# Optimization experiments

Measured on AMD Instinct MI355X. Metric: run time of the kernel, lower is better.

## Reference

```python
import jax, jax.numpy as jnp
import numpy as np

N_NODES = 100000
N_FEATURES = 128
N_FILTERS = 128
N_EDGES = 3200000


def setup_inputs() -> dict:
    key = jax.random.key(0)
    k_x, k_f, k_src, k_dst, k_w = jax.random.split(key, 5)
    x = jax.random.normal(k_x, (N_NODES, N_FEATURES), dtype=jnp.float32)
    filters = jax.random.normal(k_f, (N_FEATURES, N_FILTERS), dtype=jnp.float32)
    edge_src = jax.random.randint(k_src, (N_EDGES,), 0, N_NODES, dtype=jnp.int64)
    edge_dst = jnp.sort(jax.random.randint(k_dst, (N_EDGES,), 0, N_NODES, dtype=jnp.int64))
    edge_weight = jax.random.uniform(k_w, (N_EDGES,), dtype=jnp.float32)
    return {"x": x, "filters": filters, "edge_src": edge_src,
            "edge_dst": edge_dst, "edge_weight": edge_weight}


def reference(x, filters, edge_src, edge_dst, edge_weight):
    # Dense feature transform: XF = x @ filters  -> [N, n_filters]
    XF = jnp.matmul(x, filters)
    # Sparse aggregation: out[d] += w_e * XF[s] for each edge (s, d, w_e)
    # equivalent to torch.sparse.mm(transform, XF) with transform in COO form.
    msgs = XF[edge_src] * edge_weight[:, None]           # [E, n_filters]
    out = jax.ops.segment_sum(msgs, edge_dst, num_segments=N_NODES)
    return out
```

## Files before the change

### kernel.cpp

```cpp
#include <hip/hip_runtime.h>
#include <stdint.h>

#define N_NODES 100000
#define N_FEAT 128
#define N_EDGES 3200000

static __device__ __forceinline__ unsigned int f2bf_u(float f) {
    unsigned int u = __float_as_uint(f);
    u += 0x7FFFu + ((u >> 16) & 1u);
    return u >> 16;
}

typedef __bf16 bf16x8 __attribute__((ext_vector_type(8)));
typedef float f32x4 __attribute__((ext_vector_type(4)));

__global__ __launch_bounds__(256) void k_prep(
        const float* __restrict__ x, unsigned short* __restrict__ xi8,
        float* __restrict__ xscale,
        const float* __restrict__ f, unsigned short* __restrict__ fT,
        const int* __restrict__ dst, int* __restrict__ row_ptr) {
    int b = blockIdx.x;
    if (b < 25000) {
        int wave = threadIdx.x >> 6, lane = threadIdx.x & 63;
        int node = b * 4 + wave;
        float2 v = *(const float2*)(x + (size_t)node * 128 + lane * 2);
        float am = fmaxf(fabsf(v.x), fabsf(v.y));
        for (int d = 1; d < 64; d <<= 1) am = fmaxf(am, __shfl_xor(am, d));
        float s = am * (1.f / 127.f);
        float inv = 127.f / fmaxf(am, 1e-20f);
        int q0 = (int)rintf(v.x * inv), q1 = (int)rintf(v.y * inv);
        xi8[(size_t)node * 64 + lane] =
            (unsigned short)((q0 & 0xFF) | ((q1 & 0xFF) << 8));
        if (lane == 0) xscale[node] = s;
    } else if (b < 37500) {
        int e = (b - 25000) * 256 + threadIdx.x;
        if (e >= N_EDGES) return;
        int dcur = dst[e];
        if (e == 0) {
            for (int d = 0; d <= dcur; ++d) row_ptr[d] = 0;
        } else {
            int dprev = dst[e - 1];
            for (int d = dprev + 1; d <= dcur; ++d) row_ptr[d] = e;
        }
        if (e == N_EDGES - 1) {
            for (int d = dcur + 1; d <= N_NODES; ++d) row_ptr[d] = N_EDGES;
        }
    } else {
        int i = (b - 37500) * 256 + threadIdx.x;
        if (i >= N_FEAT * N_FEAT) return;
        int k = i >> 7, n = i & 127;
        fT[n * N_FEAT + k] = (unsigned short)f2bf_u(f[i]);
    }
}

__global__ __launch_bounds__(256) void k_aggregate(
        const unsigned int* __restrict__ xi8,
        const float* __restrict__ xscale,
        const int* __restrict__ src,
        const float* __restrict__ w,
        const int* __restrict__ row_ptr,
        unsigned int* __restrict__ aggb) {
    __shared__ uint2 smeta[4][64];
    int wave = threadIdx.x >> 6, lane = threadIdx.x & 63;
    int node = blockIdx.x * 4 + wave;
    if (node >= N_NODES) return;
    int half = lane >> 5, f = lane & 31;
    int start = row_ptr[node], end = row_ptr[node + 1];
    float a0 = 0.f, a1 = 0.f, a2 = 0.f, a3 = 0.f;

    for (int e0 = start; e0 < end; e0 += 64) {
        int e = e0 + lane;
        uint2 m = make_uint2(0u, 0u);
        if (e < end) {
            int sv = src[e];
            m.x = (unsigned int)sv;
            m.y = __float_as_uint(w[e] * xscale[sv]);
        }
        smeta[wave][lane] = m;
        int cnt16 = (min(64, end - e0) + 15) & ~15;
        for (int j = 0; j < cnt16; j += 16) {
            unsigned int vv[8]; float wj[8];
#pragma unroll
            for (int u = 0; u < 8; ++u) {
                uint2 mm = smeta[wave][j + u * 2 + half];
                wj[u] = __uint_as_float(mm.y);
                vv[u] = xi8[mm.x * 32 + f];
            }
#pragma unroll
            for (int u = 0; u < 8; ++u) {
                int s32 = (int)vv[u];
                a0 = fmaf(wj[u], (float)((s32 << 24) >> 24), a0);
                a1 = fmaf(wj[u], (float)((s32 << 16) >> 24), a1);
                a2 = fmaf(wj[u], (float)((s32 <<  8) >> 24), a2);
                a3 = fmaf(wj[u], (float)( s32        >> 24), a3);
            }
        }
    }
    a0 += __shfl_xor(a0, 32);
    a1 += __shfl_xor(a1, 32);
    a2 += __shfl_xor(a2, 32);
    a3 += __shfl_xor(a3, 32);
    if (half == 0) {
        uint2 o;
        o.x = (f2bf_u(a1) << 16) | f2bf_u(a0);
        o.y = (f2bf_u(a3) << 16) | f2bf_u(a2);
        *(uint2*)(aggb + (size_t)node * 64 + f * 2) = o;
    }
}

#define LDA 136

__global__ __launch_bounds__(256, 2) void k_gemm(
        const unsigned short* __restrict__ A,
        const unsigned short* __restrict__ BT,
        float* __restrict__ C) {
    __shared__ unsigned short Abuf[128 * LDA];
    __shared__ unsigned short Bbuf[128 * LDA];
    int t = threadIdx.x;
    int tileM = blockIdx.x * 128;

    for (int i = 0; i < 8; ++i) {
        int c = t + i * 256;
        int r = c >> 4, c8 = c & 15;
        int grow = tileM + r;
        if (grow >= N_NODES) grow = N_NODES - 1;
        uint4 va = *(const uint4*)(A + (long long)grow * 128 + c8 * 8);
        *(uint4*)(Abuf + r * LDA + c8 * 8) = va;
        uint4 vb = *(const uint4*)(BT + r * 128 + c8 * 8);
        *(uint4*)(Bbuf + r * LDA + c8 * 8) = vb;
    }
    __syncthreads();

    int wave = t >> 6, lane = t & 63;
    int wm = (wave >> 1) * 64, wn = (wave & 1) * 64;
    int m15 = lane & 15, q = lane >> 4;

    f32x4 acc[4][4];
    for (int i = 0; i < 4; ++i)
        for (int j = 0; j < 4; ++j)
            acc[i][j] = f32x4{0.f, 0.f, 0.f, 0.f};

    for (int kk = 0; kk < 128; kk += 32) {
        bf16x8 a[4], b[4];
        for (int i = 0; i < 4; ++i)
            a[i] = *(const bf16x8*)(Abuf + (wm + i * 16 + m15) * LDA + kk + q * 8);
        for (int j = 0; j < 4; ++j)
            b[j] = *(const bf16x8*)(Bbuf + (wn + j * 16 + m15) * LDA + kk + q * 8);
        for (int i = 0; i < 4; ++i)
            for (int j = 0; j < 4; ++j)
                acc[i][j] = __builtin_amdgcn_mfma_f32_16x16x32_bf16(a[i], b[j], acc[i][j], 0, 0, 0);
    }

    for (int i = 0; i < 4; ++i) {
        int rowbase = tileM + wm + i * 16 + q * 4;
        for (int j = 0; j < 4; ++j) {
            int col = wn + j * 16 + m15;
            for (int r = 0; r < 4; ++r) {
                int grow = rowbase + r;
                if (grow < N_NODES)
                    C[(long long)grow * 128 + col] = acc[i][j][r];
            }
        }
    }
}

extern "C" void kernel_launch(void* const* d_in, const int* in_sizes, int n_in,
                              void* d_out, int out_size, void* d_ws, size_t ws_size,
                              hipStream_t stream) {
    const float* x        = (const float*)d_in[0];
    const float* filters  = (const float*)d_in[1];
    const int*   edge_src = (const int*)d_in[2];
    const int*   edge_dst = (const int*)d_in[3];
    const float* edge_w   = (const float*)d_in[4];
    float* out = (float*)d_out;

    char* ws = (char*)d_ws;
    unsigned short* xi8   = (unsigned short*)(ws);
    float*          xsc   = (float*)        (ws + 13ll * 1024 * 1024);
    unsigned int*   aggb  = (unsigned int*) (ws + 14ll * 1024 * 1024);
    unsigned short* fT    = (unsigned short*)(ws + 40ll * 1024 * 1024);
    int*            rp    = (int*)          (ws + 41ll * 1024 * 1024);

    hipLaunchKernelGGL(k_prep, dim3(37564), dim3(256), 0, stream,
                       x, xi8, xsc, filters, fT, edge_dst, rp);
    hipLaunchKernelGGL(k_aggregate, dim3(25000), dim3(256), 0, stream,
                       (const unsigned int*)xi8, xsc, edge_src, edge_w, rp, aggb);
    hipLaunchKernelGGL(k_gemm, dim3(782), dim3(256), 0, stream,
                       (const unsigned short*)aggb, fT, out);
}
```

Measured before the change: 210.4 us.

## Fuse sparse aggregation with bf16 GEMM in one kernel via LDS staging

Merges the aggregation and the GEMM into one kernel. Each 512-thread block aggregates 64 nodes into a bf16 tile kept in LDS, multiplies it by the filter matrix with MFMA, and writes fp32 output through an LDS-staged, coalesced float4 store. This removes the global round trip of the aggregated intermediate and one kernel launch. The quantize prep now handles two nodes per wave with float4 loads. The cost is fewer, larger blocks, each of which must finish gathering before its GEMM starts, so occupancy and latency hiding during the gather phase may drop.

Result: slower. 232.2 us (+10.4%).

```diff
diff --git a/kernel.cpp b/kernel.cpp
--- a/kernel.cpp
+++ b/kernel.cpp
@@ -15,25 +15,27 @@
 typedef float f32x4 __attribute__((ext_vector_type(4)));
 
 __global__ __launch_bounds__(256) void k_prep(
-        const float* __restrict__ x, unsigned short* __restrict__ xi8,
+        const float* __restrict__ x, unsigned int* __restrict__ xi8,
         float* __restrict__ xscale,
         const float* __restrict__ f, unsigned short* __restrict__ fT,
         const int* __restrict__ dst, int* __restrict__ row_ptr) {
     int b = blockIdx.x;
-    if (b < 25000) {
+    if (b < 12500) {
         int wave = threadIdx.x >> 6, lane = threadIdx.x & 63;
-        int node = b * 4 + wave;
-        float2 v = *(const float2*)(x + (size_t)node * 128 + lane * 2);
-        float am = fmaxf(fabsf(v.x), fabsf(v.y));
-        for (int d = 1; d < 64; d <<= 1) am = fmaxf(am, __shfl_xor(am, d));
+        int l32 = lane & 31;
+        int node = b * 8 + wave * 2 + (lane >> 5);
+        float4 v = *(const float4*)(x + (size_t)node * 128 + l32 * 4);
+        float am = fmaxf(fmaxf(fabsf(v.x), fabsf(v.y)), fmaxf(fabsf(v.z), fabsf(v.w)));
+        for (int d = 1; d < 32; d <<= 1) am = fmaxf(am, __shfl_xor(am, d));
         float s = am * (1.f / 127.f);
         float inv = 127.f / fmaxf(am, 1e-20f);
         int q0 = (int)rintf(v.x * inv), q1 = (int)rintf(v.y * inv);
-        xi8[(size_t)node * 64 + lane] =
-            (unsigned short)((q0 & 0xFF) | ((q1 & 0xFF) << 8));
-        if (lane == 0) xscale[node] = s;
-    } else if (b < 37500) {
-        int e = (b - 25000) * 256 + threadIdx.x;
+        int q2 = (int)rintf(v.z * inv), q3 = (int)rintf(v.w * inv);
+        xi8[(size_t)node * 32 + l32] = (unsigned int)((q0 & 0xFF) | ((q1 & 0xFF) << 8) |
+                                                      ((q2 & 0xFF) << 16) | ((q3 & 0xFF) << 24));
+        if (l32 == 0) xscale[node] = s;
+    } else if (b < 25000) {
+        int e = (b - 12500) * 256 + threadIdx.x;
         if (e >= N_EDGES) return;
         int dcur = dst[e];
         if (e == 0) {
@@ -46,121 +48,111 @@
             for (int d = dcur + 1; d <= N_NODES; ++d) row_ptr[d] = N_EDGES;
         }
     } else {
-        int i = (b - 37500) * 256 + threadIdx.x;
+        int i = (b - 25000) * 256 + threadIdx.x;
         if (i >= N_FEAT * N_FEAT) return;
         int k = i >> 7, n = i & 127;
         fT[n * N_FEAT + k] = (unsigned short)f2bf_u(f[i]);
     }
 }
 
-__global__ __launch_bounds__(256) void k_aggregate(
+#define LDA 136
+#define LDC 132
+
+__global__ __launch_bounds__(512, 4) void k_agg_gemm(
         const unsigned int* __restrict__ xi8,
         const float* __restrict__ xscale,
         const int* __restrict__ src,
         const float* __restrict__ w,
         const int* __restrict__ row_ptr,
-        unsigned int* __restrict__ aggb) {
-    __shared__ uint2 smeta[4][64];
-    int wave = threadIdx.x >> 6, lane = threadIdx.x & 63;
-    int node = blockIdx.x * 4 + wave;
-    if (node >= N_NODES) return;
-    int half = lane >> 5, f = lane & 31;
-    int start = row_ptr[node], end = row_ptr[node + 1];
-    float a0 = 0.f, a1 = 0.f, a2 = 0.f, a3 = 0.f;
+        const unsigned short* __restrict__ BT,
+        float* __restrict__ C) {
+    __shared__ uint4 lds[3520];
+    uint2*          smeta = (uint2*)lds;
+    unsigned short* Abuf  = (unsigned short*)((char*)lds + 4096);
+    unsigned short* Bbuf  = (unsigned short*)((char*)lds + 4096 + 17408);
+    float*          Cbuf  = (float*)lds;
 
-    for (int e0 = start; e0 < end; e0 += 64) {
-        int e = e0 + lane;
-        uint2 m = make_uint2(0u, 0u);
-        if (e < end) {
-            int sv = src[e];
-            m.x = (unsigned int)sv;
-            m.y = __float_as_uint(w[e] * xscale[sv]);
-        }
-        smeta[wave][lane] = m;
-        int cnt16 = (min(64, end - e0) + 15) & ~15;
-        for (int j = 0; j < cnt16; j += 16) {
-            unsigned int vv[8]; float wj[8];
+    int t = threadIdx.x;
+    int wave = t >> 6, lane = t & 63;
+    int base = blockIdx.x * 64;
+
+    for (int i = 0; i < 4; ++i) {
+        int idx = t + i * 512;
+        int r = idx >> 4, c8 = idx & 15;
+        *(uint4*)(Bbuf + r * LDA + c8 * 8) = *(const uint4*)(BT + r * 128 + c8 * 8);
+    }
+
+    int half = lane >> 5, ffeat = lane & 31;
+    for (int n = 0; n < 8; ++n) {
+        int node = base + wave * 8 + n;
+        if (node >= N_NODES) break;
+        int start = row_ptr[node], end = row_ptr[node + 1];
+        float a0 = 0.f, a1 = 0.f, a2 = 0.f, a3 = 0.f;
+        for (int e0 = start; e0 < end; e0 += 64) {
+            int e = e0 + lane;
+            uint2 m = make_uint2(0u, 0u);
+            if (e < end) {
+                int sv = src[e];
+                m.x = (unsigned int)sv;
+                m.y = __float_as_uint(w[e] * xscale[sv]);
+            }
+            smeta[wave * 64 + lane] = m;
+            int cnt16 = (min(64, end - e0) + 15) & ~15;
+            for (int j = 0; j < cnt16; j += 16) {
+                unsigned int vv[8]; float wj[8];
 #pragma unroll
-            for (int u = 0; u < 8; ++u) {
-                uint2 mm = smeta[wave][j + u * 2 + half];
-                wj[u] = __uint_as_float(mm.y);
-                vv[u] = xi8[mm.x * 32 + f];
-            }
+                for (int u = 0; u < 8; ++u) {
+                    uint2 mm = smeta[wave * 64 + j + u * 2 + half];
+                    wj[u] = __uint_as_float(mm.y);
+                    vv[u] = xi8[mm.x * 32 + ffeat];
+                }
 #pragma unroll
-            for (int u = 0; u < 8; ++u) {
-                int s32 = (int)vv[u];
-                a0 = fmaf(wj[u], (float)((s32 << 24) >> 24), a0);
-                a1 = fmaf(wj[u], (float)((s32 << 16) >> 24), a1);
-                a2 = fmaf(wj[u], (float)((s32 <<  8) >> 24), a2);
-                a3 = fmaf(wj[u], (float)( s32        >> 24), a3);
+                for (int u = 0; u < 8; ++u) {
+                    int s32 = (int)vv[u];
+                    a0 = fmaf(wj[u], (float)((s32 << 24) >> 24), a0);
+                    a1 = fmaf(wj[u], (float)((s32 << 16) >> 24), a1);
+                    a2 = fmaf(wj[u], (float)((s32 <<  8) >> 24), a2);
+                    a3 = fmaf(wj[u], (float)( s32        >> 24), a3);
+                }
             }
         }
-    }
-    a0 += __shfl_xor(a0, 32);
-    a1 += __shfl_xor(a1, 32);
-    a2 += __shfl_xor(a2, 32);
-    a3 += __shfl_xor(a3, 32);
-    if (half == 0) {
-        uint2 o;
-        o.x = (f2bf_u(a1) << 16) | f2bf_u(a0);
-        o.y = (f2bf_u(a3) << 16) | f2bf_u(a2);
-        *(uint2*)(aggb + (size_t)node * 64 + f * 2) = o;
-    }
-}
-
-#define LDA 136
-
-__global__ __launch_bounds__(256, 2) void k_gemm(
-        const unsigned short* __restrict__ A,
-        const unsigned short* __restrict__ BT,
-        float* __restrict__ C) {
-    __shared__ unsigned short Abuf[128 * LDA];
-    __shared__ unsigned short Bbuf[128 * LDA];
-    int t = threadIdx.x;
-    int tileM = blockIdx.x * 128;
-
-    for (int i = 0; i < 8; ++i) {
-        int c = t + i * 256;
-        int r = c >> 4, c8 = c & 15;
-        int grow = tileM + r;
-        if (grow >= N_NODES) grow = N_NODES - 1;
-        uint4 va = *(const uint4*)(A + (long long)grow * 128 + c8 * 8);
-        *(uint4*)(Abuf + r * LDA + c8 * 8) = va;
-        uint4 vb = *(const uint4*)(BT + r * 128 + c8 * 8);
-        *(uint4*)(Bbuf + r * LDA + c8 * 8) = vb;
+        a0 += __shfl_xor(a0, 32);
+        a1 += __shfl_xor(a1, 32);
+        a2 += __shfl_xor(a2, 32);
+        a3 += __shfl_xor(a3, 32);
+        if (half == 0) {
+            uint2 o;
+            o.x = (f2bf_u(a1) << 16) | f2bf_u(a0);
+            o.y = (f2bf_u(a3) << 16) | f2bf_u(a2);
+            *(uint2*)(Abuf + (wave * 8 + n) * LDA + ffeat * 4) = o;
+        }
     }
     __syncthreads();
 
-    int wave = t >> 6, lane = t & 63;
-    int wm = (wave >> 1) * 64, wn = (wave & 1) * 64;
     int m15 = lane & 15, q = lane >> 4;
+    f32x4 acc[4];
+    for (int i = 0; i < 4; ++i) acc[i] = f32x4{0.f, 0.f, 0.f, 0.f};
+    for (int kk = 0; kk < 128; kk += 32) {
+        bf16x8 bfr = *(const bf16x8*)(Bbuf + (wave * 16 + m15) * LDA + kk + q * 8);
+#pragma unroll
+        for (int i = 0; i < 4; ++i) {
+            bf16x8 afr = *(const bf16x8*)(Abuf + (i * 16 + m15) * LDA + kk + q * 8);
+            acc[i] = __builtin_amdgcn_mfma_f32_16x16x32_bf16(afr, bfr, acc[i], 0, 0, 0);
+        }
+    }
+    __syncthreads();
 
-    f32x4 acc[4][4];
     for (int i = 0; i < 4; ++i)
-        for (int j = 0; j < 4; ++j)
-            acc[i][j] = f32x4{0.f, 0.f, 0.f, 0.f};
-
-    for (int kk = 0; kk < 128; kk += 32) {
-        bf16x8 a[4], b[4];
-        for (int i = 0; i < 4; ++i)
-            a[i] = *(const bf16x8*)(Abuf + (wm + i * 16 + m15) * LDA + kk + q * 8);
-        for (int j = 0; j < 4; ++j)
-            b[j] = *(const bf16x8*)(Bbuf + (wn + j * 16 + m15) * LDA + kk + q * 8);
-        for (int i = 0; i < 4; ++i)
-            for (int j = 0; j < 4; ++j)
-                acc[i][j] = __builtin_amdgcn_mfma_f32_16x16x32_bf16(a[i], b[j], acc[i][j], 0, 0, 0);
-    }
-
-    for (int i = 0; i < 4; ++i) {
-        int rowbase = tileM + wm + i * 16 + q * 4;
-        for (int j = 0; j < 4; ++j) {
-            int col = wn + j * 16 + m15;
-            for (int r = 0; r < 4; ++r) {
-                int grow = rowbase + r;
-                if (grow < N_NODES)
-                    C[(long long)grow * 128 + col] = acc[i][j][r];
-            }
-        }
+#pragma unroll
+        for (int r = 0; r < 4; ++r)
+            Cbuf[(i * 16 + q * 4 + r) * LDC + wave * 16 + m15] = acc[i][r];
+    __syncthreads();
+    for (int it = 0; it < 4; ++it) {
+        int idx = t + it * 512;
+        int row = idx >> 5, c4 = (idx & 31) * 4;
+        int grow = base + row;
+        if (grow < N_NODES)
+            *(float4*)(C + (size_t)grow * 128 + c4) = *(const float4*)(Cbuf + row * LDC + c4);
     }
 }
 
@@ -175,16 +167,13 @@
     float* out = (float*)d_out;
 
     char* ws = (char*)d_ws;
-    unsigned short* xi8   = (unsigned short*)(ws);
-    float*          xsc   = (float*)        (ws + 13ll * 1024 * 1024);
-    unsigned int*   aggb  = (unsigned int*) (ws + 14ll * 1024 * 1024);
-    unsigned short* fT    = (unsigned short*)(ws + 40ll * 1024 * 1024);
-    int*            rp    = (int*)          (ws + 41ll * 1024 * 1024);
+    unsigned int*   xi8  = (unsigned int*)  (ws);
+    float*          xsc  = (float*)         (ws + 13ll * 1024 * 1024);
+    unsigned short* fT   = (unsigned short*)(ws + 14ll * 1024 * 1024);
+    int*            rp   = (int*)           (ws + 15ll * 1024 * 1024);
 
-    hipLaunchKernelGGL(k_prep, dim3(37564), dim3(256), 0, stream,
+    hipLaunchKernelGGL(k_prep, dim3(25064), dim3(256), 0, stream,
                        x, xi8, xsc, filters, fT, edge_dst, rp);
-    hipLaunchKernelGGL(k_aggregate, dim3(25000), dim3(256), 0, stream,
-                       (const unsigned int*)xi8, xsc, edge_src, edge_w, rp, aggb);
-    hipLaunchKernelGGL(k_gemm, dim3(782), dim3(256), 0, stream,
-                       (const unsigned short*)aggb, fT, out);
+    hipLaunchKernelGGL(k_agg_gemm, dim3(1563), dim3(512), 0, stream,
+                       xi8, xsc, edge_src, edge_w, rp, fT, out);
 }
```
